# Performance work log

Hardware: AMD Instinct MI355X
Metric: run time of the kernel (lower is better)

The kernel has to match this reference:

```python
import jax, jax.numpy as jnp
import numpy as np

N_NODES = 100000
N_EDGES = 500000
D = 256
EPS = 0.1  # GIN epsilon applied on self-loop relation


def setup_inputs() -> dict:
    key = jax.random.key(0)
    ks = jax.random.split(key, 9)
    return {
        "x": jax.random.normal(ks[0], (N_NODES, D), dtype=jnp.float32),
        "W_self": jax.random.normal(ks[1], (D, D), dtype=jnp.float32) * 0.05,
        "W_r1": jax.random.normal(ks[2], (D, D), dtype=jnp.float32) * 0.05,
        "W_r2": jax.random.normal(ks[3], (D, D), dtype=jnp.float32) * 0.05,
        "bias": jax.random.normal(ks[4], (D,), dtype=jnp.float32) * 0.05,
        "src1": jax.random.randint(ks[5], (N_EDGES,), 0, N_NODES, dtype=jnp.int32),
        "dst1": jax.random.randint(ks[6], (N_EDGES,), 0, N_NODES, dtype=jnp.int32),
        "src2": jax.random.randint(ks[7], (N_EDGES,), 0, N_NODES, dtype=jnp.int32),
        "dst2": jax.random.randint(ks[8], (N_EDGES,), 0, N_NODES, dtype=jnp.int32),
    }


def reference(x, W_self, W_r1, W_r2, bias, src1, dst1, src2, dst2):
    # self-loop relation: features scaled by (1+eps); one self-loop edge per node
    # so copy_u + sum delivers each node exactly its own message.
    h = (1.0 + EPS) * (x @ W_self)
    # regular relations: per-node message = x @ W, gathered along src edges,
    # scatter-summed at dst (DGL fn.copy_u + fn.sum, cross-etype 'sum' reducer).
    msg1 = x @ W_r1
    h = h + jax.ops.segment_sum(msg1[src1], dst1, num_segments=N_NODES)
    msg2 = x @ W_r2
    h = h + jax.ops.segment_sum(msg2[src2], dst2, num_segments=N_NODES)
    # bias + activation, then second activation (applied twice in original);
    # mlp/batch_norm are None, dropout is identity in eval.
    h = jax.nn.relu(h + bias)
    h = jax.nn.relu(h)
    return h
```

## Files before the change

### kernel.cpp

```cpp
#include <hip/hip_runtime.h>

#define N_NODES 100000
#define N_EDGES 500000
#define D 256
#define CAP 32

typedef __bf16 bf16x8 __attribute__((ext_vector_type(8)));
typedef float  f32x4  __attribute__((ext_vector_type(4)));
typedef unsigned int u32x2 __attribute__((ext_vector_type(2)));

__device__ __forceinline__ unsigned short f2bf(float f) {
    unsigned int u = __float_as_uint(f);
    u += 0x7fffu + ((u >> 16) & 1u);
    return (unsigned short)(u >> 16);
}
__device__ __forceinline__ float bf2f(unsigned short b) {
    return __uint_as_float(((unsigned int)b) << 16);
}

#define PREP_BLOCKS 17188

__global__ __launch_bounds__(256) void prep_kernel(
    const float* __restrict__ x, unsigned short* __restrict__ xb,
    const float* __restrict__ Ws, const float* __restrict__ W1,
    const float* __restrict__ W2, unsigned short* __restrict__ Wt,
    const int* __restrict__ src1, const int* __restrict__ dst1,
    const int* __restrict__ src2, const int* __restrict__ dst2,
    int* __restrict__ cnt1, int* __restrict__ cnt2,
    int* __restrict__ bkt1, int* __restrict__ bkt2)
{
    const int wid  = blockIdx.x * 4 + (threadIdx.x >> 6);
    const int lane = threadIdx.x & 63;
    const int group = wid / 22;
    const int pos   = wid - group * 22;

    if (pos < 16) {
        int cw = group * 16 + pos;
        if (cw >= 50000) return;
        size_t i = (size_t)cw * 512 + (size_t)lane * 8;
        float4 a = *(const float4*)(x + i);
        float4 c = *(const float4*)(x + i + 4);
        union { unsigned short s[8]; uint4 u; } o;
        o.s[0] = f2bf(a.x); o.s[1] = f2bf(a.y); o.s[2] = f2bf(a.z); o.s[3] = f2bf(a.w);
        o.s[4] = f2bf(c.x); o.s[5] = f2bf(c.y); o.s[6] = f2bf(c.z); o.s[7] = f2bf(c.w);
        *(uint4*)(xb + i) = o.u;
    } else if (pos < 21) {
        int bw = group * 5 + (pos - 16);
        int e = bw * 64 + lane;
        if (e >= 2 * N_EDGES) return;
        bool r2 = (e >= N_EDGES);
        const int* src = r2 ? src2 : src1;
        const int* dst = r2 ? dst2 : dst1;
        int* cnt = r2 ? cnt2 : cnt1;
        int* bkt = r2 ? bkt2 : bkt1;
        int ei = r2 ? e - N_EDGES : e;
        int s = src[ei], d = dst[ei];
        int p = atomicAdd(&cnt[d], 1);
        if (p < CAP) bkt[d * CAP + p] = s;
    } else {
        int idx = group * 64 + lane;
        if (idx >= 3 * D * D) return;
        int k = idx >> 8;
        int n = idx & (D - 1);
        const float* W = (k < D) ? Ws : (k < 2 * D ? W1 : W2);
        float scale = (k < D) ? 1.1f : 1.0f;
        Wt[(size_t)n * (3 * D) + k] = f2bf(W[(size_t)(k & (D - 1)) * D + n] * scale);
    }
}

__global__ __launch_bounds__(256) void gather_kernel(
    const unsigned short* __restrict__ xb,
    const int* __restrict__ cnt1, const int* __restrict__ cnt2,
    const int* __restrict__ bkt1, const int* __restrict__ bkt2,
    unsigned short* __restrict__ xa1, unsigned short* __restrict__ xa2)
{
    long long gid = (long long)blockIdx.x * blockDim.x + threadIdx.x;
    int w = (int)(gid >> 6);
    int lane = (int)(gid & 63);
    if (w >= 2 * N_NODES) return;
    int node = w >> 1;
    int rel  = w & 1;

    const int* cnt = rel ? cnt2 : cnt1;
    const int* bkt = rel ? bkt2 : bkt1;
    unsigned short* xa = rel ? xa2 : xa1;

    int c = cnt[node]; if (c > CAP) c = CAP;
    int sid = (lane < c) ? bkt[(size_t)node * CAP + lane] : 0;

    ushort4 v[8];
    #pragma unroll
    for (int t = 0; t < 8; ++t) {
        int s = __shfl(sid, t);
        v[t] = *(const ushort4*)(xb + (size_t)s * D + lane * 4);
    }

    float a0 = 0.f, a1 = 0.f, a2 = 0.f, a3 = 0.f;
    #pragma unroll
    for (int t = 0; t < 8; ++t) {
        if (t < c) {
            a0 += bf2f(v[t].x); a1 += bf2f(v[t].y);
            a2 += bf2f(v[t].z); a3 += bf2f(v[t].w);
        }
    }
    for (int e = 8; e < c; ++e) {
        int s = __shfl(sid, e);
        ushort4 t = *(const ushort4*)(xb + (size_t)s * D + lane * 4);
        a0 += bf2f(t.x); a1 += bf2f(t.y); a2 += bf2f(t.z); a3 += bf2f(t.w);
    }

    u32x2 o;
    o.x = (unsigned)f2bf(a0) | ((unsigned)f2bf(a1) << 16);
    o.y = (unsigned)f2bf(a2) | ((unsigned)f2bf(a3) << 16);
    __builtin_nontemporal_store(o, (u32x2*)(xa + (size_t)node * D + lane * 4));
}

__global__ __launch_bounds__(512) void gemm_kernel(
    const unsigned short* __restrict__ xb,
    const unsigned short* __restrict__ xa1,
    const unsigned short* __restrict__ xa2,
    const unsigned short* __restrict__ Wt,
    const float* __restrict__ bias, float* __restrict__ out)
{
    __shared__ unsigned short Alds[128 * 32];
    __shared__ unsigned short Blds[256 * 32];

    const int tid  = threadIdx.x;
    const int lane = tid & 63;
    const int wave = tid >> 6;
    const int quad = lane >> 4;
    const int l15  = lane & 15;
    const int m0 = blockIdx.x * 128;
    const int wm = (wave >> 2) * 64;
    const int wn = (wave & 3) * 64;

    const unsigned short* Aseg[3] = {xb, xa1, xa2};

    const int rowA = tid >> 2, kqA = tid & 3;
    int mA = m0 + rowA; if (mA >= N_NODES) mA = N_NODES - 1;
    const int wAoff  = rowA * 32 + ((kqA ^ ((rowA >> 1) & 3)) * 8);
    const int nB0 = tid >> 2, nB1 = nB0 + 128;
    const int wB0off = nB0 * 32 + ((kqA ^ ((nB0 >> 1) & 3)) * 8);
    const int wB1off = nB1 * 32 + ((kqA ^ ((nB1 >> 1) & 3)) * 8);
    const int swz = (l15 >> 1) & 3;

    f32x4 acc[4][4] = {};

    uint4 ra  = *(const uint4*)(Aseg[0] + (size_t)mA * D + kqA * 8);
    uint4 rb0 = *(const uint4*)(Wt + (size_t)nB0 * (3 * D) + kqA * 8);
    uint4 rb1 = *(const uint4*)(Wt + (size_t)nB1 * (3 * D) + kqA * 8);

    for (int kt = 0; kt < 24; ++kt) {
        *(uint4*)(Alds + wAoff) = ra;
        *(uint4*)(Blds + wB0off) = rb0;
        *(uint4*)(Blds + wB1off) = rb1;
        __syncthreads();

        if (kt + 1 < 24) {
            const unsigned short* __restrict__ An = Aseg[(kt + 1) >> 3];
            const int kon = ((kt + 1) & 7) * 32;
            ra  = *(const uint4*)(An + (size_t)mA * D + kon + kqA * 8);
            rb0 = *(const uint4*)(Wt + (size_t)nB0 * (3 * D) + (kt + 1) * 32 + kqA * 8);
            rb1 = *(const uint4*)(Wt + (size_t)nB1 * (3 * D) + (kt + 1) * 32 + kqA * 8);
        }

        bf16x8 af[4], bfr[4];
        #pragma unroll
        for (int i = 0; i < 4; ++i) {
            af[i]  = *(const bf16x8*)(Alds + (wm + i * 16 + l15) * 32 + ((quad ^ swz) * 8));
            bfr[i] = *(const bf16x8*)(Blds + (wn + i * 16 + l15) * 32 + ((quad ^ swz) * 8));
        }
        #pragma unroll
        for (int i = 0; i < 4; ++i)
            #pragma unroll
            for (int j = 0; j < 4; ++j)
                acc[i][j] = __builtin_amdgcn_mfma_f32_16x16x32_bf16(
                    af[i], bfr[j], acc[i][j], 0, 0, 0);
        __syncthreads();
    }

    #pragma unroll
    for (int j = 0; j < 4; ++j) {
        int col = wn + j * 16 + l15;
        float bj = bias[col];
        #pragma unroll
        for (int i = 0; i < 4; ++i) {
            int rb = m0 + wm + i * 16 + quad * 4;
            #pragma unroll
            for (int r = 0; r < 4; ++r) {
                int m = rb + r;
                if (m < N_NODES)
                    __builtin_nontemporal_store(
                        fmaxf(acc[i][j][r] + bj, 0.f),
                        out + (size_t)m * D + col);
            }
        }
    }
}

extern "C" void kernel_launch(void* const* d_in, const int* in_sizes, int n_in,
                              void* d_out, int out_size, void* d_ws, size_t ws_size,
                              hipStream_t stream) {
    const float* x    = (const float*)d_in[0];
    const float* Ws   = (const float*)d_in[1];
    const float* W1   = (const float*)d_in[2];
    const float* W2   = (const float*)d_in[3];
    const float* bias = (const float*)d_in[4];
    const int* src1   = (const int*)d_in[5];
    const int* dst1   = (const int*)d_in[6];
    const int* src2   = (const int*)d_in[7];
    const int* dst2   = (const int*)d_in[8];
    float* out = (float*)d_out;

    char* p = (char*)d_ws;
    unsigned short* xb  = (unsigned short*)p; p += (size_t)N_NODES * D * 2;
    unsigned short* xa1 = (unsigned short*)p; p += (size_t)N_NODES * D * 2;
    unsigned short* xa2 = (unsigned short*)p; p += (size_t)N_NODES * D * 2;
    int* cnt1 = (int*)p; p += (size_t)N_NODES * 4;
    int* cnt2 = (int*)p; p += (size_t)N_NODES * 4;
    int* bkt1 = (int*)p; p += (size_t)N_NODES * CAP * 4;
    int* bkt2 = (int*)p; p += (size_t)N_NODES * CAP * 4;
    unsigned short* Wt = (unsigned short*)p;

    (void)hipMemsetAsync(cnt1, 0, (size_t)2 * N_NODES * 4, stream);

    prep_kernel<<<PREP_BLOCKS, 256, 0, stream>>>(
        x, xb, Ws, W1, W2, Wt, src1, dst1, src2, dst2, cnt1, cnt2, bkt1, bkt2);

    {
        long long total = (long long)2 * N_NODES * 64;
        gather_kernel<<<(int)((total + 255) / 256), 256, 0, stream>>>(
            xb, cnt1, cnt2, bkt1, bkt2, xa1, xa2);
    }
    {
        gemm_kernel<<<(N_NODES + 127) / 128, 512, 0, stream>>>(
            xb, xa1, xa2, Wt, bias, out);
    }
}
```

Baseline: 406.7 us.

## Fuse neighbor gather-sum into GEMM A-tile loads, dropping aggregate buffers

Removes the separate gather kernel and the xa1/xa2 intermediate buffers. The GEMM now stages each block's bucket IDs in LDS and, for the two relation k-segments, gathers neighbor bf16 rows directly while loading A. The gathered sums are accumulated in registers and packed into the A tile, overlapping with the MFMAs. This saves a kernel launch and the write plus re-read of two 51 MB aggregate arrays. In exchange the GEMM holds more registers and LDS (32 KB of IDs, 4-block launch bound), which may cut occupancy or stall on the irregular gathers.

```diff
diff --git a/kernel.cpp b/kernel.cpp
--- a/kernel.cpp
+++ b/kernel.cpp
@@ -7,7 +7,6 @@
 
 typedef __bf16 bf16x8 __attribute__((ext_vector_type(8)));
 typedef float  f32x4  __attribute__((ext_vector_type(4)));
-typedef unsigned int u32x2 __attribute__((ext_vector_type(2)));
 
 __device__ __forceinline__ unsigned short f2bf(float f) {
     unsigned int u = __float_as_uint(f);
@@ -17,6 +16,8 @@
 __device__ __forceinline__ float bf2f(unsigned short b) {
     return __uint_as_float(((unsigned int)b) << 16);
 }
+__device__ __forceinline__ float bfu_lo(unsigned u) { return __uint_as_float(u << 16); }
+__device__ __forceinline__ float bfu_hi(unsigned u) { return __uint_as_float(u & 0xffff0000u); }
 
 #define PREP_BLOCKS 17188
 
@@ -68,62 +69,16 @@
     }
 }
 
-__global__ __launch_bounds__(256) void gather_kernel(
+__global__ __launch_bounds__(512, 4) void gemm_kernel(
     const unsigned short* __restrict__ xb,
     const int* __restrict__ cnt1, const int* __restrict__ cnt2,
     const int* __restrict__ bkt1, const int* __restrict__ bkt2,
-    unsigned short* __restrict__ xa1, unsigned short* __restrict__ xa2)
-{
-    long long gid = (long long)blockIdx.x * blockDim.x + threadIdx.x;
-    int w = (int)(gid >> 6);
-    int lane = (int)(gid & 63);
-    if (w >= 2 * N_NODES) return;
-    int node = w >> 1;
-    int rel  = w & 1;
-
-    const int* cnt = rel ? cnt2 : cnt1;
-    const int* bkt = rel ? bkt2 : bkt1;
-    unsigned short* xa = rel ? xa2 : xa1;
-
-    int c = cnt[node]; if (c > CAP) c = CAP;
-    int sid = (lane < c) ? bkt[(size_t)node * CAP + lane] : 0;
-
-    ushort4 v[8];
-    #pragma unroll
-    for (int t = 0; t < 8; ++t) {
-        int s = __shfl(sid, t);
-        v[t] = *(const ushort4*)(xb + (size_t)s * D + lane * 4);
-    }
-
-    float a0 = 0.f, a1 = 0.f, a2 = 0.f, a3 = 0.f;
-    #pragma unroll
-    for (int t = 0; t < 8; ++t) {
-        if (t < c) {
-            a0 += bf2f(v[t].x); a1 += bf2f(v[t].y);
-            a2 += bf2f(v[t].z); a3 += bf2f(v[t].w);
-        }
-    }
-    for (int e = 8; e < c; ++e) {
-        int s = __shfl(sid, e);
-        ushort4 t = *(const ushort4*)(xb + (size_t)s * D + lane * 4);
-        a0 += bf2f(t.x); a1 += bf2f(t.y); a2 += bf2f(t.z); a3 += bf2f(t.w);
-    }
-
-    u32x2 o;
-    o.x = (unsigned)f2bf(a0) | ((unsigned)f2bf(a1) << 16);
-    o.y = (unsigned)f2bf(a2) | ((unsigned)f2bf(a3) << 16);
-    __builtin_nontemporal_store(o, (u32x2*)(xa + (size_t)node * D + lane * 4));
-}
-
-__global__ __launch_bounds__(512) void gemm_kernel(
-    const unsigned short* __restrict__ xb,
-    const unsigned short* __restrict__ xa1,
-    const unsigned short* __restrict__ xa2,
     const unsigned short* __restrict__ Wt,
     const float* __restrict__ bias, float* __restrict__ out)
 {
     __shared__ unsigned short Alds[128 * 32];
     __shared__ unsigned short Blds[256 * 32];
+    __shared__ int idsL[2 * 128 * CAP];
 
     const int tid  = threadIdx.x;
     const int lane = tid & 63;
@@ -134,8 +89,6 @@
     const int wm = (wave >> 2) * 64;
     const int wn = (wave & 3) * 64;
 
-    const unsigned short* Aseg[3] = {xb, xa1, xa2};
-
     const int rowA = tid >> 2, kqA = tid & 3;
     int mA = m0 + rowA; if (mA >= N_NODES) mA = N_NODES - 1;
     const int wAoff  = rowA * 32 + ((kqA ^ ((rowA >> 1) & 3)) * 8);
@@ -144,38 +97,119 @@
     const int wB1off = nB1 * 32 + ((kqA ^ ((nB1 >> 1) & 3)) * 8);
     const int swz = (l15 >> 1) & 3;
 
+    {
+        int rel = tid >> 8;
+        int n   = (tid & 255) >> 1;
+        int h   = (tid & 1) << 4;
+        int nc  = m0 + n; if (nc >= N_NODES) nc = N_NODES - 1;
+        const int* bsrc = (rel ? bkt2 : bkt1) + (size_t)nc * CAP + h;
+        int* ldst = idsL + rel * (128 * CAP) + n * CAP + h;
+        uint4 b0 = *(const uint4*)(bsrc + 0);
+        uint4 b1 = *(const uint4*)(bsrc + 4);
+        uint4 b2 = *(const uint4*)(bsrc + 8);
+        uint4 b3 = *(const uint4*)(bsrc + 12);
+        *(uint4*)(ldst + 0)  = b0;
+        *(uint4*)(ldst + 4)  = b1;
+        *(uint4*)(ldst + 8)  = b2;
+        *(uint4*)(ldst + 12) = b3;
+    }
+
+    int c1 = cnt1[mA]; if (c1 > CAP) c1 = CAP;
+    int c2 = cnt2[mA]; if (c2 > CAP) c2 = CAP;
+    const int* myids1 = idsL + rowA * CAP;
+    const int* myids2 = idsL + (128 * CAP) + rowA * CAP;
+
     f32x4 acc[4][4] = {};
 
-    uint4 ra  = *(const uint4*)(Aseg[0] + (size_t)mA * D + kqA * 8);
+    uint4 ra  = *(const uint4*)(xb + (size_t)mA * D + kqA * 8);
     uint4 rb0 = *(const uint4*)(Wt + (size_t)nB0 * (3 * D) + kqA * 8);
     uint4 rb1 = *(const uint4*)(Wt + (size_t)nB1 * (3 * D) + kqA * 8);
 
+    uint4 gv[8];
+
     for (int kt = 0; kt < 24; ++kt) {
-        *(uint4*)(Alds + wAoff) = ra;
+        *(uint4*)(Alds + wAoff)  = ra;
         *(uint4*)(Blds + wB0off) = rb0;
         *(uint4*)(Blds + wB1off) = rb1;
         __syncthreads();
 
-        if (kt + 1 < 24) {
-            const unsigned short* __restrict__ An = Aseg[(kt + 1) >> 3];
-            const int kon = ((kt + 1) & 7) * 32;
-            ra  = *(const uint4*)(An + (size_t)mA * D + kon + kqA * 8);
-            rb0 = *(const uint4*)(Wt + (size_t)nB0 * (3 * D) + (kt + 1) * 32 + kqA * 8);
-            rb1 = *(const uint4*)(Wt + (size_t)nB1 * (3 * D) + (kt + 1) * 32 + kqA * 8);
-        }
-
-        bf16x8 af[4], bfr[4];
+        const int ktn = kt + 1;
+        int cc = 0;
+        const int* myids = myids1;
+        if (ktn < 24) {
+            if (ktn < 8) {
+                ra = *(const uint4*)(xb + (size_t)mA * D + ktn * 32 + kqA * 8);
+            } else {
+                const bool r2g = (ktn >= 16);
+                cc    = r2g ? c2 : c1;
+                myids = r2g ? myids2 : myids1;
+                const int ks = (ktn - 8) & 7;
+                const unsigned short* gbase = xb + ks * 32 + kqA * 8;
+                #pragma unroll
+                for (int e = 0; e < 8; ++e) {
+                    if (e < cc) {
+                        int s = myids[e];
+                        gv[e] = *(const uint4*)(gbase + (size_t)s * D);
+                    }
+                }
+            }
+            rb0 = *(const uint4*)(Wt + (size_t)nB0 * (3 * D) + ktn * 32 + kqA * 8);
+            rb1 = *(const uint4*)(Wt + (size_t)nB1 * (3 * D) + ktn * 32 + kqA * 8);
+        }
+
+        bf16x8 b0f = *(const bf16x8*)(Blds + (wn +  0 + l15) * 32 + ((quad ^ swz) * 8));
+        bf16x8 b1f = *(const bf16x8*)(Blds + (wn + 16 + l15) * 32 + ((quad ^ swz) * 8));
+        bf16x8 b2f = *(const bf16x8*)(Blds + (wn + 32 + l15) * 32 + ((quad ^ swz) * 8));
+        bf16x8 b3f = *(const bf16x8*)(Blds + (wn + 48 + l15) * 32 + ((quad ^ swz) * 8));
         #pragma unroll
         for (int i = 0; i < 4; ++i) {
-            af[i]  = *(const bf16x8*)(Alds + (wm + i * 16 + l15) * 32 + ((quad ^ swz) * 8));
-            bfr[i] = *(const bf16x8*)(Blds + (wn + i * 16 + l15) * 32 + ((quad ^ swz) * 8));
-        }
-        #pragma unroll
-        for (int i = 0; i < 4; ++i)
+            bf16x8 afi = *(const bf16x8*)(Alds + (wm + i * 16 + l15) * 32 + ((quad ^ swz) * 8));
+            acc[i][0] = __builtin_amdgcn_mfma_f32_16x16x32_bf16(afi, b0f, acc[i][0], 0, 0, 0);
+            acc[i][1] = __builtin_amdgcn_mfma_f32_16x16x32_bf16(afi, b1f, acc[i][1], 0, 0, 0);
+            acc[i][2] = __builtin_amdgcn_mfma_f32_16x16x32_bf16(afi, b2f, acc[i][2], 0, 0, 0);
+            acc[i][3] = __builtin_amdgcn_mfma_f32_16x16x32_bf16(afi, b3f, acc[i][3], 0, 0, 0);
+        }
+
+        if (ktn >= 8 && ktn < 24) {
+            const int ks = (ktn - 8) & 7;
+            float s0 = 0.f, s1 = 0.f, s2 = 0.f, s3 = 0.f;
+            float s4 = 0.f, s5 = 0.f, s6 = 0.f, s7 = 0.f;
             #pragma unroll
-            for (int j = 0; j < 4; ++j)
-                acc[i][j] = __builtin_amdgcn_mfma_f32_16x16x32_bf16(
-                    af[i], bfr[j], acc[i][j], 0, 0, 0);
+            for (int e = 0; e < 8; ++e) {
+                if (e < cc) {
+                    s0 += bfu_lo(gv[e].x); s1 += bfu_hi(gv[e].x);
+                    s2 += bfu_lo(gv[e].y); s3 += bfu_hi(gv[e].y);
+                    s4 += bfu_lo(gv[e].z); s5 += bfu_hi(gv[e].z);
+                    s6 += bfu_lo(gv[e].w); s7 += bfu_hi(gv[e].w);
+                }
+            }
+            if (cc > 8) {
+                const unsigned short* gbase = xb + ks * 32 + kqA * 8;
+                uint4 tv[8];
+                #pragma unroll
+                for (int e = 8; e < 16; ++e)
+                    if (e < cc) tv[e - 8] = *(const uint4*)(gbase + (size_t)myids[e] * D);
+                #pragma unroll
+                for (int e = 8; e < 16; ++e)
+                    if (e < cc) {
+                        s0 += bfu_lo(tv[e-8].x); s1 += bfu_hi(tv[e-8].x);
+                        s2 += bfu_lo(tv[e-8].y); s3 += bfu_hi(tv[e-8].y);
+                        s4 += bfu_lo(tv[e-8].z); s5 += bfu_hi(tv[e-8].z);
+                        s6 += bfu_lo(tv[e-8].w); s7 += bfu_hi(tv[e-8].w);
+                    }
+                for (int e = 16; e < cc; ++e) {
+                    uint4 t = *(const uint4*)(gbase + (size_t)myids[e] * D);
+                    s0 += bfu_lo(t.x); s1 += bfu_hi(t.x);
+                    s2 += bfu_lo(t.y); s3 += bfu_hi(t.y);
+                    s4 += bfu_lo(t.z); s5 += bfu_hi(t.z);
+                    s6 += bfu_lo(t.w); s7 += bfu_hi(t.w);
+                }
+            }
+            ra.x = (unsigned)f2bf(s0) | ((unsigned)f2bf(s1) << 16);
+            ra.y = (unsigned)f2bf(s2) | ((unsigned)f2bf(s3) << 16);
+            ra.z = (unsigned)f2bf(s4) | ((unsigned)f2bf(s5) << 16);
+            ra.w = (unsigned)f2bf(s6) | ((unsigned)f2bf(s7) << 16);
+        }
         __syncthreads();
     }
 
@@ -214,8 +248,6 @@
 
     char* p = (char*)d_ws;
     unsigned short* xb  = (unsigned short*)p; p += (size_t)N_NODES * D * 2;
-    unsigned short* xa1 = (unsigned short*)p; p += (size_t)N_NODES * D * 2;
-    unsigned short* xa2 = (unsigned short*)p; p += (size_t)N_NODES * D * 2;
     int* cnt1 = (int*)p; p += (size_t)N_NODES * 4;
     int* cnt2 = (int*)p; p += (size_t)N_NODES * 4;
     int* bkt1 = (int*)p; p += (size_t)N_NODES * CAP * 4;
@@ -227,13 +259,6 @@
     prep_kernel<<<PREP_BLOCKS, 256, 0, stream>>>(
         x, xb, Ws, W1, W2, Wt, src1, dst1, src2, dst2, cnt1, cnt2, bkt1, bkt2);
 
-    {
-        long long total = (long long)2 * N_NODES * 64;
-        gather_kernel<<<(int)((total + 255) / 256), 256, 0, stream>>>(
-            xb, cnt1, cnt2, bkt1, bkt2, xa1, xa2);
-    }
-    {
-        gemm_kernel<<<(N_NODES + 127) / 128, 512, 0, stream>>>(
-            xb, xa1, xa2, Wt, bias, out);
-    }
-}
+    gemm_kernel<<<(N_NODES + 127) / 128, 512, 0, stream>>>(
+        xb, cnt1, cnt2, bkt1, bkt2, Wt, bias, out);
+}
```

New measurement: 853.8 us. 110% more time.

## Double-buffer GEMM tiles via direct global-to-LDS loads with pre-swizzled weights

Applied to the files above, without the earlier changes.

The GEMM now loads A and B tiles with global_load_lds straight into a double-buffered LDS region, replacing the register staging and second barrier per k-step. To keep the XOR swizzle with a direct copy, the weight transpose in prep now writes Wt already swizzled and the A row offsets carry the swizzle. The prep x conversion is also restructured into two half-row ushort4 stores, and launch bounds request 4 blocks per CU. This doubles LDS use and relies on the compiler inserting correct waits for the async LDS loads before the barrier.

```diff
diff --git a/kernel.cpp b/kernel.cpp
--- a/kernel.cpp
+++ b/kernel.cpp
@@ -4,6 +4,7 @@
 #define N_EDGES 500000
 #define D 256
 #define CAP 32
+#define BM 128
 
 typedef __bf16 bf16x8 __attribute__((ext_vector_type(8)));
 typedef float  f32x4  __attribute__((ext_vector_type(4)));
@@ -16,6 +17,13 @@
 }
 __device__ __forceinline__ float bf2f(unsigned short b) {
     return __uint_as_float(((unsigned int)b) << 16);
+}
+
+__device__ __forceinline__ void glds16(const unsigned short* g, unsigned short* l) {
+    __builtin_amdgcn_global_load_lds(
+        (const __attribute__((address_space(1))) unsigned int*)g,
+        (__attribute__((address_space(3))) unsigned int*)l,
+        16, 0, 0);
 }
 
 #define PREP_BLOCKS 17188
@@ -37,13 +45,14 @@
     if (pos < 16) {
         int cw = group * 16 + pos;
         if (cw >= 50000) return;
-        size_t i = (size_t)cw * 512 + (size_t)lane * 8;
-        float4 a = *(const float4*)(x + i);
-        float4 c = *(const float4*)(x + i + 4);
-        union { unsigned short s[8]; uint4 u; } o;
-        o.s[0] = f2bf(a.x); o.s[1] = f2bf(a.y); o.s[2] = f2bf(a.z); o.s[3] = f2bf(a.w);
-        o.s[4] = f2bf(c.x); o.s[5] = f2bf(c.y); o.s[6] = f2bf(c.z); o.s[7] = f2bf(c.w);
-        *(uint4*)(xb + i) = o.u;
+        size_t base = (size_t)cw * 512;
+        float4 a = *(const float4*)(x + base + lane * 4);
+        float4 c = *(const float4*)(x + base + 256 + lane * 4);
+        ushort4 oa, oc;
+        oa.x = f2bf(a.x); oa.y = f2bf(a.y); oa.z = f2bf(a.z); oa.w = f2bf(a.w);
+        oc.x = f2bf(c.x); oc.y = f2bf(c.y); oc.z = f2bf(c.z); oc.w = f2bf(c.w);
+        *(ushort4*)(xb + base + lane * 4) = oa;
+        *(ushort4*)(xb + base + 256 + lane * 4) = oc;
     } else if (pos < 21) {
         int bw = group * 5 + (pos - 16);
         int e = bw * 64 + lane;
@@ -64,7 +73,8 @@
         int n = idx & (D - 1);
         const float* W = (k < D) ? Ws : (k < 2 * D ? W1 : W2);
         float scale = (k < D) ? 1.1f : 1.0f;
-        Wt[(size_t)n * (3 * D) + k] = f2bf(W[(size_t)(k & (D - 1)) * D + n] * scale);
+        int dk = k ^ ((((n >> 1) & 3)) << 3);
+        Wt[(size_t)n * (3 * D) + dk] = f2bf(W[(size_t)(k & (D - 1)) * D + n] * scale);
     }
 }
 
@@ -115,67 +125,65 @@
     __builtin_nontemporal_store(o, (u32x2*)(xa + (size_t)node * D + lane * 4));
 }
 
-__global__ __launch_bounds__(512) void gemm_kernel(
+__global__ __launch_bounds__(512, 4) void gemm_kernel(
     const unsigned short* __restrict__ xb,
     const unsigned short* __restrict__ xa1,
     const unsigned short* __restrict__ xa2,
     const unsigned short* __restrict__ Wt,
     const float* __restrict__ bias, float* __restrict__ out)
 {
-    __shared__ unsigned short Alds[128 * 32];
-    __shared__ unsigned short Blds[256 * 32];
+    __shared__ unsigned short Alds[2][BM * 32];
+    __shared__ unsigned short Blds[2][256 * 32];
 
     const int tid  = threadIdx.x;
     const int lane = tid & 63;
     const int wave = tid >> 6;
     const int quad = lane >> 4;
     const int l15  = lane & 15;
-    const int m0 = blockIdx.x * 128;
+    const int m0 = blockIdx.x * BM;
     const int wm = (wave >> 2) * 64;
     const int wn = (wave & 3) * 64;
-
+    const int swz = (l15 >> 1) & 3;
+
+    const int gr   = lane >> 2;
+    const int gch  = lane & 3;
+    const int gswz = (lane >> 3) & 3;
+    int mRow = m0 + (wave << 4) + gr;
+    if (mRow >= N_NODES) mRow = N_NODES - 1;
+    const size_t aRowOff = (size_t)mRow * D + ((gch ^ gswz) << 3);
+    const unsigned short* bSrc0 = Wt + (size_t)((wave << 4) + gr) * (3 * D) + (gch << 3);
+    const unsigned short* bSrc1 = bSrc0 + (size_t)128 * (3 * D);
     const unsigned short* Aseg[3] = {xb, xa1, xa2};
 
-    const int rowA = tid >> 2, kqA = tid & 3;
-    int mA = m0 + rowA; if (mA >= N_NODES) mA = N_NODES - 1;
-    const int wAoff  = rowA * 32 + ((kqA ^ ((rowA >> 1) & 3)) * 8);
-    const int nB0 = tid >> 2, nB1 = nB0 + 128;
-    const int wB0off = nB0 * 32 + ((kqA ^ ((nB0 >> 1) & 3)) * 8);
-    const int wB1off = nB1 * 32 + ((kqA ^ ((nB1 >> 1) & 3)) * 8);
-    const int swz = (l15 >> 1) & 3;
-
     f32x4 acc[4][4] = {};
 
-    uint4 ra  = *(const uint4*)(Aseg[0] + (size_t)mA * D + kqA * 8);
-    uint4 rb0 = *(const uint4*)(Wt + (size_t)nB0 * (3 * D) + kqA * 8);
-    uint4 rb1 = *(const uint4*)(Wt + (size_t)nB1 * (3 * D) + kqA * 8);
+    glds16(Aseg[0] + aRowOff, &Alds[0][wave * 512]);
+    glds16(bSrc0, &Blds[0][wave * 512]);
+    glds16(bSrc1, &Blds[0][4096 + wave * 512]);
+    __syncthreads();
 
     for (int kt = 0; kt < 24; ++kt) {
-        *(uint4*)(Alds + wAoff) = ra;
-        *(uint4*)(Blds + wB0off) = rb0;
-        *(uint4*)(Blds + wB1off) = rb1;
-        __syncthreads();
-
-        if (kt + 1 < 24) {
-            const unsigned short* __restrict__ An = Aseg[(kt + 1) >> 3];
-            const int kon = ((kt + 1) & 7) * 32;
-            ra  = *(const uint4*)(An + (size_t)mA * D + kon + kqA * 8);
-            rb0 = *(const uint4*)(Wt + (size_t)nB0 * (3 * D) + (kt + 1) * 32 + kqA * 8);
-            rb1 = *(const uint4*)(Wt + (size_t)nB1 * (3 * D) + (kt + 1) * 32 + kqA * 8);
-        }
-
-        bf16x8 af[4], bfr[4];
+        const int ktn = kt + 1;
+        if (ktn < 24) {
+            glds16(Aseg[ktn >> 3] + aRowOff + ((ktn & 7) * 32), &Alds[ktn & 1][wave * 512]);
+            glds16(bSrc0 + ktn * 32, &Blds[ktn & 1][wave * 512]);
+            glds16(bSrc1 + ktn * 32, &Blds[ktn & 1][4096 + wave * 512]);
+        }
+
+        const unsigned short* Ab = &Alds[kt & 1][0];
+        const unsigned short* Bb = &Blds[kt & 1][0];
+        bf16x8 b0f = *(const bf16x8*)(Bb + (wn +  0 + l15) * 32 + ((quad ^ swz) * 8));
+        bf16x8 b1f = *(const bf16x8*)(Bb + (wn + 16 + l15) * 32 + ((quad ^ swz) * 8));
+        bf16x8 b2f = *(const bf16x8*)(Bb + (wn + 32 + l15) * 32 + ((quad ^ swz) * 8));
+        bf16x8 b3f = *(const bf16x8*)(Bb + (wn + 48 + l15) * 32 + ((quad ^ swz) * 8));
         #pragma unroll
         for (int i = 0; i < 4; ++i) {
-            af[i]  = *(const bf16x8*)(Alds + (wm + i * 16 + l15) * 32 + ((quad ^ swz) * 8));
-            bfr[i] = *(const bf16x8*)(Blds + (wn + i * 16 + l15) * 32 + ((quad ^ swz) * 8));
-        }
-        #pragma unroll
-        for (int i = 0; i < 4; ++i)
-            #pragma unroll
-            for (int j = 0; j < 4; ++j)
-                acc[i][j] = __builtin_amdgcn_mfma_f32_16x16x32_bf16(
-                    af[i], bfr[j], acc[i][j], 0, 0, 0);
+            bf16x8 afi = *(const bf16x8*)(Ab + (wm + i * 16 + l15) * 32 + ((quad ^ swz) * 8));
+            acc[i][0] = __builtin_amdgcn_mfma_f32_16x16x32_bf16(afi, b0f, acc[i][0], 0, 0, 0);
+            acc[i][1] = __builtin_amdgcn_mfma_f32_16x16x32_bf16(afi, b1f, acc[i][1], 0, 0, 0);
+            acc[i][2] = __builtin_amdgcn_mfma_f32_16x16x32_bf16(afi, b2f, acc[i][2], 0, 0, 0);
+            acc[i][3] = __builtin_amdgcn_mfma_f32_16x16x32_bf16(afi, b3f, acc[i][3], 0, 0, 0);
+        }
         __syncthreads();
     }
 
@@ -233,7 +241,7 @@
             xb, cnt1, cnt2, bkt1, bkt2, xa1, xa2);
     }
     {
-        gemm_kernel<<<(N_NODES + 127) / 128, 512, 0, stream>>>(
+        gemm_kernel<<<(N_NODES + BM - 1) / BM, 512, 0, stream>>>(
             xb, xa1, xa2, Wt, bias, out);
     }
 }
```

After: 393.6 us. -3.2%, faster.
